# Performance work log

Measured on AMD Instinct MI355X. Metric: run time of the kernel, lower is better.

The kernel has to match this reference:

```python
import jax, jax.numpy as jnp
import numpy as np

T, D_IN, D_OUT, R, S = 8192, 4096, 4096, 16, 16  # tokens, in, out, lora rank, n_stacks
GATE_THRESHOLD = 0.12


def setup_inputs() -> dict:
    key = jax.random.key(0)
    ks = jax.random.split(key, 6)
    x = jax.random.normal(ks[0], (T, D_IN), jnp.float32)
    W = jax.random.normal(ks[1], (D_OUT, D_IN), jnp.float32) * 0.02  # frozen linear weight
    b = jax.random.normal(ks[2], (D_OUT,), jnp.float32) * 0.02       # frozen linear bias
    A = jax.random.normal(ks[3], (S, R, D_IN), jnp.float32) * 0.02   # per-stack lora_A
    B = jax.random.normal(ks[4], (S, D_OUT, R), jnp.float32) * 0.02  # per-stack lora_B
    domain_weights = jax.random.uniform(ks[5], (S,), jnp.float32)    # sigmoid-router weights per domain
    stack_domain = jnp.arange(S, dtype=jnp.int32)                    # stack -> domain index (count=1 each)
    return {"x": x, "W": W, "b": b, "A": A, "B": B,
            "domain_weights": domain_weights, "stack_domain": stack_domain}


def reference(x, W, b, A, B, domain_weights, stack_domain):
    # base frozen linear: out = x @ W^T + b
    base = x @ W.T + b  # [T, D_OUT]
    # threshold-gated per-stack weights: w if w > GATE_THRESHOLD else 0
    g = jnp.where(domain_weights > GATE_THRESHOLD, domain_weights, 0.0)[stack_domain]  # [S]
    # grouped LoRA: stack(x) = (x @ A_s^T) @ B_s^T, combined with gate weights
    h = jnp.einsum('td,srd->str', x, A)          # [S, T, R]
    lora = jnp.einsum('s,str,sor->to', g, h, B)  # [T, D_OUT]
    # original wraps stack contributions in torch.no_grad()
    return base + jax.lax.stop_gradient(lora)
```

## Files before the change

### kernel.cpp

```cpp
#include <hip/hip_runtime.h>
#include <hip/hip_bf16.h>

typedef __bf16 bf16;
typedef __attribute__((ext_vector_type(8))) __bf16 bf16x8;
typedef __attribute__((ext_vector_type(4))) float f32x4;
typedef __attribute__((ext_vector_type(16))) float f32x16;

#define T_TOK 8192
#define DIN   4096
#define DOUT  4096
#define RNK   16
#define NS    16
#define KLORA (NS * RNK)
#define GATE  0.12f

typedef __attribute__((address_space(1))) const void gconst_t;
typedef __attribute__((address_space(3))) void lds_t;

__device__ __forceinline__ void gload_lds16(const void* g, void* l) {
  __builtin_amdgcn_global_load_lds((gconst_t*)g, (lds_t*)l, 16, 0, 0);
}

#define BAR() do { asm volatile("" ::: "memory"); \
                   __builtin_amdgcn_s_barrier();  \
                   asm volatile("" ::: "memory"); } while (0)
#define VMW(n) asm volatile("s_waitcnt vmcnt(" #n ")" ::: "memory")
#define LGKM(n) do { asm volatile("s_waitcnt lgkmcnt(" #n ")" ::: "memory"); \
                     __builtin_amdgcn_sched_barrier(0); } while (0)
#define SB0 __builtin_amdgcn_sched_barrier(0)

__global__ __launch_bounds__(256)
void prep_all_kernel(const float* __restrict__ x, bf16* __restrict__ xb,
                     const float* __restrict__ B, const float* __restrict__ dw,
                     const int* __restrict__ sd, bf16* __restrict__ bg,
                     const float* __restrict__ A, bf16* __restrict__ at) {
  __shared__ float tl[32][33];
  const int bid = blockIdx.x;
  if (bid < 16384) {
    const long i = ((long)bid * 256 + threadIdx.x) * 8;
    const float4 v0 = *(const float4*)(x + i);
    const float4 v1 = *(const float4*)(x + i + 4);
    bf16x8 o;
    o[0] = (bf16)v0.x; o[1] = (bf16)v0.y; o[2] = (bf16)v0.z; o[3] = (bf16)v0.w;
    o[4] = (bf16)v1.x; o[5] = (bf16)v1.y; o[6] = (bf16)v1.z; o[7] = (bf16)v1.w;
    *(bf16x8*)(xb + i) = o;
  } else if (bid < 16384 + 4096) {
    const int t = (bid - 16384) * 256 + threadIdx.x;
    const int o = t >> 8, k = t & 255, s = k >> 4, r = k & 15;
    const float w = dw[sd[s]];
    const float g = (w > GATE) ? w : 0.f;
    bg[t] = (bf16)(g * B[((size_t)s * DOUT + o) * RNK + r]);
  } else {
    const int tb = bid - 16384 - 4096;
    const int d0 = (tb & 127) * 32, k0 = (tb >> 7) * 32;
    const int tx = threadIdx.x & 31, ty = threadIdx.x >> 5;
#pragma unroll
    for (int i = 0; i < 32; i += 8)
      tl[ty + i][tx] = A[(size_t)(k0 + ty + i) * DIN + d0 + tx];
    __syncthreads();
#pragma unroll
    for (int i = 0; i < 32; i += 8)
      at[(size_t)(d0 + ty + i) * KLORA + k0 + tx] = (bf16)tl[tx][ty + i];
  }
}

__global__ __launch_bounds__(256)
void gemm_bt(const bf16* __restrict__ Am, const bf16* __restrict__ Bm,
             const float* __restrict__ extra, bf16* __restrict__ outB,
             int M, int N, int K) {
  constexpr int BM = 128, BN = 128, BK = 32;
  __shared__ __align__(16) bf16 At[BM * BK];
  __shared__ __align__(16) bf16 Bt[BN * BK];

  const int tid  = threadIdx.x;
  const int wave = tid >> 6, lane = tid & 63;

  const int nwg = gridDim.x, bid = blockIdx.x;
  const int qq  = nwg >> 3;
  const int sw  = (bid & 7) * qq + (bid >> 3);
  const int ntN = N / BN;
  const long row0 = (long)(sw / ntN) * BM;
  const long col0 = (long)(sw % ntN) * BN;

  f32x4 acc[4][4] = {};
  const int kSteps = K / BK;

  auto stage = [&](int ks) {
    const long k0 = (long)ks * BK;
#pragma unroll
    for (int r = 0; r < 2; ++r) {
      const int off = tid * 16 + r * 4096;
      const int row = off >> 6;
      const int el  = (off & 63) >> 1;
      char* ldsA = (char*)At + (wave << 10) + (r << 12);
      char* ldsB = (char*)Bt + (wave << 10) + (r << 12);
      gload_lds16(Am + (row0 + row) * K + k0 + el, ldsA);
      gload_lds16(Bm + (col0 + row) * K + k0 + el, ldsB);
    }
  };

  stage(0);
  for (int ks = 0; ks < kSteps; ++ks) {
    __syncthreads();
    bf16x8 afr[4], bfr[4];
    const int koff = (lane >> 4) << 3;
    const int rsel = lane & 15;
    const int wr = wave >> 1, wc = wave & 1;
#pragma unroll
    for (int m = 0; m < 4; ++m)
      afr[m] = *(const bf16x8*)&At[((wr << 6) + (m << 4) + rsel) * BK + koff];
#pragma unroll
    for (int n = 0; n < 4; ++n)
      bfr[n] = *(const bf16x8*)&Bt[((wc << 6) + (n << 4) + rsel) * BK + koff];
    __syncthreads();
    if (ks + 1 < kSteps) stage(ks + 1);
#pragma unroll
    for (int m = 0; m < 4; ++m)
#pragma unroll
      for (int n = 0; n < 4; ++n)
        acc[m][n] = __builtin_amdgcn_mfma_f32_16x16x32_bf16(afr[m], bfr[n],
                                                            acc[m][n], 0, 0, 0);
  }

  const int wr = wave >> 1, wc = wave & 1;
#pragma unroll
  for (int m = 0; m < 4; ++m)
#pragma unroll
    for (int n = 0; n < 4; ++n)
#pragma unroll
      for (int j = 0; j < 4; ++j) {
        const long row = row0 + wr * 64 + m * 16 + ((lane >> 4) << 2) + j;
        const long col = col0 + wc * 64 + n * 16 + (lane & 15);
        outB[row * N + col] = (bf16)(acc[m][n][j] + extra[row * N + col]);
      }
}

__global__ __launch_bounds__(512, 2)
void gemm256(const bf16* __restrict__ Am, const bf16* __restrict__ Bm,
             const float* __restrict__ bias, float* __restrict__ out,
             int M, int N, int K) {
  extern __shared__ char smem[];
  const int tid  = threadIdx.x;
  const int wave = tid >> 6, lane = tid & 63;
  const int wr = wave >> 2, wc = wave & 3;
  const int lane31 = lane & 31, kh = lane >> 5;

  const int nwg = gridDim.x, bid = blockIdx.x;
  const int sw  = (bid & 7) * (nwg >> 3) + (bid >> 3);
  const int ntN = N >> 8;
  const long row0 = (long)(sw / ntN) << 8;
  const long col0 = (long)(sw % ntN) << 8;

  long srcA[2], srcB[2];
  int  ldsd[2];
#pragma unroll
  for (int r = 0; r < 2; ++r) {
    const int row = wave * 32 + r * 16 + (lane >> 2);
    const int kbe = ((((lane & 3) * 16) ^ ((lane & 32) >> 1) ^ (r << 5)) >> 1);
    srcA[r] = (row0 + row) * (long)K + kbe;
    srcB[r] = (col0 + row) * (long)K + kbe;
    ldsd[r] = (wave * 2 + r) << 10;
  }

  const int nT = K >> 6;

  auto stage_half = [&](int H) {
    if (H >= 4 * nT) return;
    const int  slot = H & 7;
    const long kofs = (long)(H >> 2) * 64 + (long)((H >> 1) & 1) * 32;
    if (H & 1) {
#pragma unroll
      for (int r = 0; r < 2; ++r)
        gload_lds16(Bm + srcB[r] + kofs, smem + (slot << 14) + ldsd[r]);
    } else {
#pragma unroll
      for (int r = 0; r < 2; ++r)
        gload_lds16(Am + srcA[r] + kofs, smem + (slot << 14) + ldsd[r]);
    }
  };

  const int swz = (lane & 24) << 1;
  int lo32[2];
  lo32[0] = lane31 * 64 + (((0 * 2 + kh) * 16) ^ swz);
  lo32[1] = lane31 * 64 + (((1 * 2 + kh) * 16) ^ swz);

  f32x16 acc32[4][2] = {};
  bf16x8 afr0[2][2], afr1[2][2], bfr0[2][2], bfr1[2][2];

#define RDA32(slot, mh, mi, kst, dst) \
  (dst)[(mi)][(kst)] = *(const bf16x8*)(smem + ((slot) << 14) + \
      (((wr << 7) + (mh) * 64 + (mi) * 32) << 6) + lo32[(kst)])
#define RDB32(slot, n, kst, dst) \
  (dst)[(n)][(kst)] = *(const bf16x8*)(smem + ((slot) << 14) + \
      (((wc << 6) + (n) * 32) << 6) + lo32[(kst)])
#define MB32(mh, mi, n, kst, A_, B_) \
  acc32[(mh) * 2 + (mi)][(n)] = __builtin_amdgcn_mfma_f32_32x32x16_bf16( \
      (A_)[(mi)][(kst)], (B_)[(n)][(kst)], acc32[(mh) * 2 + (mi)][(n)], 0, 0, 0)

  stage_half(0); stage_half(1); stage_half(2); stage_half(3); stage_half(4);
  VMW(6);
  BAR();
  RDB32(1, 0, 0, bfr0); RDB32(1, 0, 1, bfr0);
  RDB32(1, 1, 0, bfr0); RDB32(1, 1, 1, bfr0);
  RDA32(0, 0, 0, 0, afr0); RDA32(0, 0, 0, 1, afr0);
  RDA32(0, 0, 1, 0, afr0); RDA32(0, 0, 1, 1, afr0);

  for (int t = 0; t < nT; ++t) {
    const int b  = (t & 1) << 2;
    const int b2 = b ^ 4;
    const bool last = (t == nT - 1);
    BAR();
    stage_half(4 * t + 5);
    LGKM(0);
    __builtin_amdgcn_s_setprio(1);
    MB32(0, 0, 0, 0, afr0, bfr0); MB32(0, 0, 1, 0, afr0, bfr0); SB0; RDA32(b | 0, 1, 0, 0, afr1); SB0;
    MB32(0, 1, 0, 0, afr0, bfr0); MB32(0, 1, 1, 0, afr0, bfr0); SB0; RDA32(b | 0, 1, 1, 0, afr1); SB0;
    MB32(0, 0, 0, 1, afr0, bfr0); MB32(0, 0, 1, 1, afr0, bfr0); SB0; RDA32(b | 0, 1, 0, 1, afr1); SB0;
    MB32(0, 1, 0, 1, afr0, bfr0); MB32(0, 1, 1, 1, afr0, bfr0); SB0; RDA32(b | 0, 1, 1, 1, afr1);
    __builtin_amdgcn_s_setprio(0);
    if (last) { VMW(0); } else { VMW(4); }
    BAR();
    stage_half(4 * t + 6);
    LGKM(0);
    __builtin_amdgcn_s_setprio(1);
    MB32(1, 0, 0, 0, afr1, bfr0); MB32(1, 0, 1, 0, afr1, bfr0); SB0; RDB32(b | 3, 0, 0, bfr1); RDB32(b | 3, 0, 1, bfr1); SB0;
    MB32(1, 1, 0, 0, afr1, bfr0); MB32(1, 1, 1, 0, afr1, bfr0); SB0; RDB32(b | 3, 1, 0, bfr1); RDB32(b | 3, 1, 1, bfr1); SB0;
    MB32(1, 0, 0, 1, afr1, bfr0); MB32(1, 0, 1, 1, afr1, bfr0); SB0; RDA32(b | 2, 0, 0, 0, afr0); RDA32(b | 2, 0, 0, 1, afr0); SB0;
    MB32(1, 1, 0, 1, afr1, bfr0); MB32(1, 1, 1, 1, afr1, bfr0); SB0; RDA32(b | 2, 0, 1, 0, afr0); RDA32(b | 2, 0, 1, 1, afr0);
    __builtin_amdgcn_s_setprio(0);
    BAR();
    stage_half(4 * t + 7);
    LGKM(0);
    __builtin_amdgcn_s_setprio(1);
    MB32(0, 0, 0, 0, afr0, bfr1); MB32(0, 0, 1, 0, afr0, bfr1); SB0; RDA32(b | 2, 1, 0, 0, afr1); SB0;
    MB32(0, 1, 0, 0, afr0, bfr1); MB32(0, 1, 1, 0, afr0, bfr1); SB0; RDA32(b | 2, 1, 1, 0, afr1); SB0;
    MB32(0, 0, 0, 1, afr0, bfr1); MB32(0, 0, 1, 1, afr0, bfr1); SB0; RDA32(b | 2, 1, 0, 1, afr1); SB0;
    MB32(0, 1, 0, 1, afr0, bfr1); MB32(0, 1, 1, 1, afr0, bfr1); SB0; RDA32(b | 2, 1, 1, 1, afr1);
    __builtin_amdgcn_s_setprio(0);
    VMW(4);
    BAR();
    stage_half(4 * t + 8);
    LGKM(0);
    __builtin_amdgcn_s_setprio(1);
    if (!last) {
      MB32(1, 0, 0, 0, afr1, bfr1); MB32(1, 0, 1, 0, afr1, bfr1); SB0; RDB32(b2 | 1, 0, 0, bfr0); RDB32(b2 | 1, 0, 1, bfr0); SB0;
      MB32(1, 1, 0, 0, afr1, bfr1); MB32(1, 1, 1, 0, afr1, bfr1); SB0; RDB32(b2 | 1, 1, 0, bfr0); RDB32(b2 | 1, 1, 1, bfr0); SB0;
      MB32(1, 0, 0, 1, afr1, bfr1); MB32(1, 0, 1, 1, afr1, bfr1); SB0; RDA32(b2 | 0, 0, 0, 0, afr0); RDA32(b2 | 0, 0, 0, 1, afr0); SB0;
      MB32(1, 1, 0, 1, afr1, bfr1); MB32(1, 1, 1, 1, afr1, bfr1); SB0; RDA32(b2 | 0, 0, 1, 0, afr0); RDA32(b2 | 0, 0, 1, 1, afr0);
    } else {
      MB32(1, 0, 0, 0, afr1, bfr1); MB32(1, 0, 1, 0, afr1, bfr1);
      MB32(1, 1, 0, 0, afr1, bfr1); MB32(1, 1, 1, 0, afr1, bfr1);
      MB32(1, 0, 0, 1, afr1, bfr1); MB32(1, 0, 1, 1, afr1, bfr1);
      MB32(1, 1, 0, 1, afr1, bfr1); MB32(1, 1, 1, 1, afr1, bfr1);
    }
    __builtin_amdgcn_s_setprio(0);
  }

#undef RDA32
#undef RDB32
#undef MB32

#pragma unroll
  for (int mi4 = 0; mi4 < 4; ++mi4)
#pragma unroll
    for (int n = 0; n < 2; ++n)
#pragma unroll
      for (int reg = 0; reg < 16; ++reg) {
        const long row = row0 + wr * 128 + mi4 * 32 + (reg & 3) + ((reg >> 2) << 3) + (kh << 2);
        const long col = col0 + wc * 64 + n * 32 + lane31;
        out[row * N + col] = acc32[mi4][n][reg] + bias[col];
      }
}


extern "C" void kernel_launch(void* const* d_in, const int* in_sizes, int n_in,
                              void* d_out, int out_size, void* d_ws, size_t ws_size,
                              hipStream_t stream) {
  (void)in_sizes; (void)n_in; (void)out_size; (void)ws_size;
  const float* x  = (const float*)d_in[0];
  const float* W  = (const float*)d_in[1];
  const float* b  = (const float*)d_in[2];
  const float* A  = (const float*)d_in[3];
  const float* B  = (const float*)d_in[4];
  const float* dw = (const float*)d_in[5];
  const int*   sd = (const int*)d_in[6];
  float* out = (float*)d_out;

  char* ws = (char*)d_ws;
  bf16* xb    = (bf16*)(ws);
  bf16* weff  = (bf16*)(ws + ((size_t)64 << 20));
  bf16* bg    = (bf16*)(ws + ((size_t)96 << 20));
  bf16* acatT = (bf16*)(ws + ((size_t)98 << 20));

  prep_all_kernel<<<16384 + 4096 + 1024, 256, 0, stream>>>(
      x, xb, B, dw, sd, bg, A, acatT);

  gemm_bt<<<(DOUT / 128) * (DIN / 128), 256, 0, stream>>>(
      bg, acatT, W, weff, DOUT, DIN, KLORA);

  static_assert((T_TOK % 256) == 0 && (DOUT % 256) == 0 && (DIN % 64) == 0, "");
  hipFuncSetAttribute(reinterpret_cast<const void*>(gemm256),
                      hipFuncAttributeMaxDynamicSharedMemorySize, 131072);
  gemm256<<<(T_TOK / 256) * (DOUT / 256), 512, 131072, stream>>>(
      xb, weff, b, out, T_TOK, DOUT, DIN);
}
```

Before: 325.6 us.

## Use 4 waves per 256x256 tile with 128x128 per-wave subtiles

Reworks the main GEMM from 8 waves (2x4, 128x64 each) to 4 waves (2x2, 128x128 each) per 256x256 tile. Each wave issues twice as many global->LDS loads and B-fragment reads, and accumulates 16 32x32 MFMA tiles. This raises per-wave arithmetic intensity and cuts LDS read traffic per FLOP. The cost is much higher register pressure (256 accumulator floats) and fewer waves to hide latency.

```diff
diff --git a/kernel.cpp b/kernel.cpp
--- a/kernel.cpp
+++ b/kernel.cpp
@@ -135,14 +135,14 @@
       }
 }
 
-__global__ __launch_bounds__(512, 2)
+__global__ __launch_bounds__(256, 1)
 void gemm256(const bf16* __restrict__ Am, const bf16* __restrict__ Bm,
              const float* __restrict__ bias, float* __restrict__ out,
              int M, int N, int K) {
   extern __shared__ char smem[];
   const int tid  = threadIdx.x;
   const int wave = tid >> 6, lane = tid & 63;
-  const int wr = wave >> 2, wc = wave & 3;
+  const int wr = wave >> 1, wc = wave & 1;
   const int lane31 = lane & 31, kh = lane >> 5;
 
   const int nwg = gridDim.x, bid = blockIdx.x;
@@ -151,15 +151,15 @@
   const long row0 = (long)(sw / ntN) << 8;
   const long col0 = (long)(sw % ntN) << 8;
 
-  long srcA[2], srcB[2];
-  int  ldsd[2];
-#pragma unroll
-  for (int r = 0; r < 2; ++r) {
-    const int row = wave * 32 + r * 16 + (lane >> 2);
-    const int kbe = ((((lane & 3) * 16) ^ ((lane & 32) >> 1) ^ (r << 5)) >> 1);
+  long srcA[4], srcB[4];
+  int  ldsd[4];
+#pragma unroll
+  for (int r = 0; r < 4; ++r) {
+    const int row = (wave * 4 + r) * 16 + (lane >> 2);
+    const int kbe = ((((lane & 3) * 16) ^ ((lane & 32) >> 1) ^ ((r & 1) << 5)) >> 1);
     srcA[r] = (row0 + row) * (long)K + kbe;
     srcB[r] = (col0 + row) * (long)K + kbe;
-    ldsd[r] = (wave * 2 + r) << 10;
+    ldsd[r] = (wave * 4 + r) << 10;
   }
 
   const int nT = K >> 6;
@@ -170,11 +170,11 @@
     const long kofs = (long)(H >> 2) * 64 + (long)((H >> 1) & 1) * 32;
     if (H & 1) {
 #pragma unroll
-      for (int r = 0; r < 2; ++r)
+      for (int r = 0; r < 4; ++r)
         gload_lds16(Bm + srcB[r] + kofs, smem + (slot << 14) + ldsd[r]);
     } else {
 #pragma unroll
-      for (int r = 0; r < 2; ++r)
+      for (int r = 0; r < 4; ++r)
         gload_lds16(Am + srcA[r] + kofs, smem + (slot << 14) + ldsd[r]);
     }
   };
@@ -184,24 +184,31 @@
   lo32[0] = lane31 * 64 + (((0 * 2 + kh) * 16) ^ swz);
   lo32[1] = lane31 * 64 + (((1 * 2 + kh) * 16) ^ swz);
 
-  f32x16 acc32[4][2] = {};
-  bf16x8 afr0[2][2], afr1[2][2], bfr0[2][2], bfr1[2][2];
-
-#define RDA32(slot, mh, mi, kst, dst) \
-  (dst)[(mi)][(kst)] = *(const bf16x8*)(smem + ((slot) << 14) + \
-      (((wr << 7) + (mh) * 64 + (mi) * 32) << 6) + lo32[(kst)])
+  f32x16 acc32[4][4] = {};
+  bf16x8 afr0[2][2], afr1[2][2];
+  bf16x8 bfr0[4][2], bfr1[4][2];
+
+#define RDA32(slot, mh, mi2, kst, dst) \
+  (dst)[(mi2)][(kst)] = *(const bf16x8*)(smem + ((slot) << 14) + \
+      (((wr * 128) + (mh) * 64 + (mi2) * 32) << 6) + lo32[(kst)])
 #define RDB32(slot, n, kst, dst) \
   (dst)[(n)][(kst)] = *(const bf16x8*)(smem + ((slot) << 14) + \
-      (((wc << 6) + (n) * 32) << 6) + lo32[(kst)])
-#define MB32(mh, mi, n, kst, A_, B_) \
-  acc32[(mh) * 2 + (mi)][(n)] = __builtin_amdgcn_mfma_f32_32x32x16_bf16( \
-      (A_)[(mi)][(kst)], (B_)[(n)][(kst)], acc32[(mh) * 2 + (mi)][(n)], 0, 0, 0)
+      (((wc * 128) + (n) * 32) << 6) + lo32[(kst)])
+#define MB32(mh, mi2, n, kst, A_, B_) \
+  acc32[(mh) * 2 + (mi2)][(n)] = __builtin_amdgcn_mfma_f32_32x32x16_bf16( \
+      (A_)[(mi2)][(kst)], (B_)[(n)][(kst)], acc32[(mh) * 2 + (mi2)][(n)], 0, 0, 0)
+#define MG4(mh, mi2, kst, A_, B_) do { \
+  MB32(mh, mi2, 0, kst, A_, B_); MB32(mh, mi2, 1, kst, A_, B_); \
+  MB32(mh, mi2, 2, kst, A_, B_); MB32(mh, mi2, 3, kst, A_, B_); \
+} while (0)
 
   stage_half(0); stage_half(1); stage_half(2); stage_half(3); stage_half(4);
-  VMW(6);
+  VMW(12);
   BAR();
   RDB32(1, 0, 0, bfr0); RDB32(1, 0, 1, bfr0);
   RDB32(1, 1, 0, bfr0); RDB32(1, 1, 1, bfr0);
+  RDB32(1, 2, 0, bfr0); RDB32(1, 2, 1, bfr0);
+  RDB32(1, 3, 0, bfr0); RDB32(1, 3, 1, bfr0);
   RDA32(0, 0, 0, 0, afr0); RDA32(0, 0, 0, 1, afr0);
   RDA32(0, 0, 1, 0, afr0); RDA32(0, 0, 1, 1, afr0);
 
@@ -213,45 +220,43 @@
     stage_half(4 * t + 5);
     LGKM(0);
     __builtin_amdgcn_s_setprio(1);
-    MB32(0, 0, 0, 0, afr0, bfr0); MB32(0, 0, 1, 0, afr0, bfr0); SB0; RDA32(b | 0, 1, 0, 0, afr1); SB0;
-    MB32(0, 1, 0, 0, afr0, bfr0); MB32(0, 1, 1, 0, afr0, bfr0); SB0; RDA32(b | 0, 1, 1, 0, afr1); SB0;
-    MB32(0, 0, 0, 1, afr0, bfr0); MB32(0, 0, 1, 1, afr0, bfr0); SB0; RDA32(b | 0, 1, 0, 1, afr1); SB0;
-    MB32(0, 1, 0, 1, afr0, bfr0); MB32(0, 1, 1, 1, afr0, bfr0); SB0; RDA32(b | 0, 1, 1, 1, afr1);
+    MG4(0, 0, 0, afr0, bfr0); SB0; RDA32(b | 0, 1, 0, 0, afr1); SB0;
+    MG4(0, 1, 0, afr0, bfr0); SB0; RDA32(b | 0, 1, 1, 0, afr1); SB0;
+    MG4(0, 0, 1, afr0, bfr0); SB0; RDA32(b | 0, 1, 0, 1, afr1); SB0;
+    MG4(0, 1, 1, afr0, bfr0); SB0; RDA32(b | 0, 1, 1, 1, afr1);
     __builtin_amdgcn_s_setprio(0);
-    if (last) { VMW(0); } else { VMW(4); }
+    if (last) { VMW(0); } else { VMW(8); }
     BAR();
     stage_half(4 * t + 6);
     LGKM(0);
     __builtin_amdgcn_s_setprio(1);
-    MB32(1, 0, 0, 0, afr1, bfr0); MB32(1, 0, 1, 0, afr1, bfr0); SB0; RDB32(b | 3, 0, 0, bfr1); RDB32(b | 3, 0, 1, bfr1); SB0;
-    MB32(1, 1, 0, 0, afr1, bfr0); MB32(1, 1, 1, 0, afr1, bfr0); SB0; RDB32(b | 3, 1, 0, bfr1); RDB32(b | 3, 1, 1, bfr1); SB0;
-    MB32(1, 0, 0, 1, afr1, bfr0); MB32(1, 0, 1, 1, afr1, bfr0); SB0; RDA32(b | 2, 0, 0, 0, afr0); RDA32(b | 2, 0, 0, 1, afr0); SB0;
-    MB32(1, 1, 0, 1, afr1, bfr0); MB32(1, 1, 1, 1, afr1, bfr0); SB0; RDA32(b | 2, 0, 1, 0, afr0); RDA32(b | 2, 0, 1, 1, afr0);
+    MG4(1, 0, 0, afr1, bfr0); SB0; RDB32(b | 3, 0, 0, bfr1); RDB32(b | 3, 0, 1, bfr1); RDB32(b | 3, 1, 0, bfr1); SB0;
+    MG4(1, 1, 0, afr1, bfr0); SB0; RDB32(b | 3, 1, 1, bfr1); RDB32(b | 3, 2, 0, bfr1); RDB32(b | 3, 2, 1, bfr1); SB0;
+    MG4(1, 0, 1, afr1, bfr0); SB0; RDB32(b | 3, 3, 0, bfr1); RDB32(b | 3, 3, 1, bfr1); RDA32(b | 2, 0, 0, 0, afr0); SB0;
+    MG4(1, 1, 1, afr1, bfr0); SB0; RDA32(b | 2, 0, 0, 1, afr0); RDA32(b | 2, 0, 1, 0, afr0); RDA32(b | 2, 0, 1, 1, afr0);
     __builtin_amdgcn_s_setprio(0);
     BAR();
     stage_half(4 * t + 7);
     LGKM(0);
     __builtin_amdgcn_s_setprio(1);
-    MB32(0, 0, 0, 0, afr0, bfr1); MB32(0, 0, 1, 0, afr0, bfr1); SB0; RDA32(b | 2, 1, 0, 0, afr1); SB0;
-    MB32(0, 1, 0, 0, afr0, bfr1); MB32(0, 1, 1, 0, afr0, bfr1); SB0; RDA32(b | 2, 1, 1, 0, afr1); SB0;
-    MB32(0, 0, 0, 1, afr0, bfr1); MB32(0, 0, 1, 1, afr0, bfr1); SB0; RDA32(b | 2, 1, 0, 1, afr1); SB0;
-    MB32(0, 1, 0, 1, afr0, bfr1); MB32(0, 1, 1, 1, afr0, bfr1); SB0; RDA32(b | 2, 1, 1, 1, afr1);
+    MG4(0, 0, 0, afr0, bfr1); SB0; RDA32(b | 2, 1, 0, 0, afr1); SB0;
+    MG4(0, 1, 0, afr0, bfr1); SB0; RDA32(b | 2, 1, 1, 0, afr1); SB0;
+    MG4(0, 0, 1, afr0, bfr1); SB0; RDA32(b | 2, 1, 0, 1, afr1); SB0;
+    MG4(0, 1, 1, afr0, bfr1); SB0; RDA32(b | 2, 1, 1, 1, afr1);
     __builtin_amdgcn_s_setprio(0);
-    VMW(4);
+    VMW(8);
     BAR();
     stage_half(4 * t + 8);
     LGKM(0);
     __builtin_amdgcn_s_setprio(1);
     if (!last) {
-      MB32(1, 0, 0, 0, afr1, bfr1); MB32(1, 0, 1, 0, afr1, bfr1); SB0; RDB32(b2 | 1, 0, 0, bfr0); RDB32(b2 | 1, 0, 1, bfr0); SB0;
-      MB32(1, 1, 0, 0, afr1, bfr1); MB32(1, 1, 1, 0, afr1, bfr1); SB0; RDB32(b2 | 1, 1, 0, bfr0); RDB32(b2 | 1, 1, 1, bfr0); SB0;
-      MB32(1, 0, 0, 1, afr1, bfr1); MB32(1, 0, 1, 1, afr1, bfr1); SB0; RDA32(b2 | 0, 0, 0, 0, afr0); RDA32(b2 | 0, 0, 0, 1, afr0); SB0;
-      MB32(1, 1, 0, 1, afr1, bfr1); MB32(1, 1, 1, 1, afr1, bfr1); SB0; RDA32(b2 | 0, 0, 1, 0, afr0); RDA32(b2 | 0, 0, 1, 1, afr0);
+      MG4(1, 0, 0, afr1, bfr1); SB0; RDB32(b2 | 1, 0, 0, bfr0); RDB32(b2 | 1, 0, 1, bfr0); RDB32(b2 | 1, 1, 0, bfr0); SB0;
+      MG4(1, 1, 0, afr1, bfr1); SB0; RDB32(b2 | 1, 1, 1, bfr0); RDB32(b2 | 1, 2, 0, bfr0); RDB32(b2 | 1, 2, 1, bfr0); SB0;
+      MG4(1, 0, 1, afr1, bfr1); SB0; RDB32(b2 | 1, 3, 0, bfr0); RDB32(b2 | 1, 3, 1, bfr0); RDA32(b2 | 0, 0, 0, 0, afr0); SB0;
+      MG4(1, 1, 1, afr1, bfr1); SB0; RDA32(b2 | 0, 0, 0, 1, afr0); RDA32(b2 | 0, 0, 1, 0, afr0); RDA32(b2 | 0, 0, 1, 1, afr0);
     } else {
-      MB32(1, 0, 0, 0, afr1, bfr1); MB32(1, 0, 1, 0, afr1, bfr1);
-      MB32(1, 1, 0, 0, afr1, bfr1); MB32(1, 1, 1, 0, afr1, bfr1);
-      MB32(1, 0, 0, 1, afr1, bfr1); MB32(1, 0, 1, 1, afr1, bfr1);
-      MB32(1, 1, 0, 1, afr1, bfr1); MB32(1, 1, 1, 1, afr1, bfr1);
+      MG4(1, 0, 0, afr1, bfr1); MG4(1, 1, 0, afr1, bfr1);
+      MG4(1, 0, 1, afr1, bfr1); MG4(1, 1, 1, afr1, bfr1);
     }
     __builtin_amdgcn_s_setprio(0);
   }
@@ -259,15 +264,16 @@
 #undef RDA32
 #undef RDB32
 #undef MB32
+#undef MG4
 
 #pragma unroll
   for (int mi4 = 0; mi4 < 4; ++mi4)
 #pragma unroll
-    for (int n = 0; n < 2; ++n)
+    for (int n = 0; n < 4; ++n)
 #pragma unroll
       for (int reg = 0; reg < 16; ++reg) {
         const long row = row0 + wr * 128 + mi4 * 32 + (reg & 3) + ((reg >> 2) << 3) + (kh << 2);
-        const long col = col0 + wc * 64 + n * 32 + lane31;
+        const long col = col0 + wc * 128 + n * 32 + lane31;
         out[row * N + col] = acc32[mi4][n][reg] + bias[col];
       }
 }
@@ -301,6 +307,6 @@
   static_assert((T_TOK % 256) == 0 && (DOUT % 256) == 0 && (DIN % 64) == 0, "");
   hipFuncSetAttribute(reinterpret_cast<const void*>(gemm256),
                       hipFuncAttributeMaxDynamicSharedMemorySize, 131072);
-  gemm256<<<(T_TOK / 256) * (DOUT / 256), 512, 131072, stream>>>(
+  gemm256<<<(T_TOK / 256) * (DOUT / 256), 256, 131072, stream>>>(
       xb, weff, b, out, T_TOK, DOUT, DIN);
 }
```

Measured after the change: 328.5 us. Within noise of the previous version (+0.9%).
